# Kernel optimization log

Measured on AMD Instinct MI355X. Metric: run time of the kernel, lower is better.

## Reference

```python
import jax, jax.numpy as jnp
import numpy as np

N_NODES = 100000
N_EDGES = 3200000
IN_DIM = 3
HID = 8
OUT_DIM = 1


def setup_inputs() -> dict:
    key = jax.random.key(0)
    ks = jax.random.split(key, 10)
    x = jax.random.normal(ks[0], (N_NODES, IN_DIM), dtype=jnp.float32)
    edge_index = jax.random.randint(ks[1], (2, N_EDGES), 0, N_NODES, dtype=jnp.int64)
    cat_dim = 2 * (HID + IN_DIM)  # 22
    s = lambda fan_in: 1.0 / np.sqrt(fan_in)
    W_in = jax.random.uniform(ks[2], (IN_DIM, HID), jnp.float32, -s(IN_DIM), s(IN_DIM))
    b_in = jnp.zeros((HID,), jnp.float32)
    W1 = jax.random.uniform(ks[3], (cat_dim, HID), jnp.float32, -s(cat_dim), s(cat_dim))
    b1 = jnp.zeros((HID,), jnp.float32)
    W2 = jax.random.uniform(ks[4], (HID, HID), jnp.float32, -s(HID), s(HID))
    b2 = jnp.zeros((HID,), jnp.float32)
    W_e = jax.random.uniform(ks[5], (cat_dim, OUT_DIM), jnp.float32, -s(cat_dim), s(cat_dim))
    b_e = jnp.zeros((OUT_DIM,), jnp.float32)
    return {"x": x, "edge_index": edge_index, "W_in": W_in, "b_in": b_in,
            "W1": W1, "b1": b1, "W2": W2, "b2": b2, "W_e": W_e, "b_e": b_e}


def reference(x, edge_index, W_in, b_in, W1, b1, W2, b2, W_e, b_e):
    src = edge_index[0]  # j (source)
    dst = edge_index[1]  # i (target)

    # inputnet: Linear + Tanh
    H = jnp.tanh(x @ W_in + b_in)               # [N, HID]
    feat = jnp.concatenate([H, x], axis=-1)      # [N, HID+IN_DIM]

    # One EdgeConv iteration (n_iters=1): message = nn(cat([x_i, x_j - x_i]))
    xi = feat[dst]                                # [E, 11]
    xj = feat[src]                                # [E, 11]
    e = jnp.concatenate([xi, xj - xi], axis=-1)   # [E, 22]
    m = jax.nn.sigmoid(e @ W1 + b1)               # [E, HID]
    m = jax.nn.sigmoid(m @ W2 + b2)               # [E, HID]
    H = jax.ops.segment_sum(m, dst, num_segments=N_NODES)  # scatter-add to targets
    feat = jnp.concatenate([H, x], axis=-1)       # [N, 11]

    # edgenetwork on concatenated endpoint features
    ef = jnp.concatenate([feat[src], feat[dst]], axis=-1)   # [E, 22]
    out = jax.nn.sigmoid(ef @ W_e + b_e)          # [E, 1]
    return out.squeeze(-1)                        # [E]
```

## Files before the change

kernel.cpp:

```cpp
#include <hip/hip_runtime.h>
#include <hip/hip_fp16.h>

#define TPB     256
#define BSH     9
#define BW      512
#define EPB     8192
#define NBMAX   256
#define MAXNB   1024
#define S_SPLIT 8

static __device__ __forceinline__ float sigmoidf(float v) {
    return __builtin_amdgcn_rcpf(1.0f + __expf(-v));
}

static __device__ __forceinline__ void ldgj(const __half* __restrict__ gjh, int n,
                                            float o[8]) {
    uint4 u = *(const uint4*)(gjh + (size_t)n * 8);
    union { unsigned int u; __half2 h; } c0, c1, c2, c3;
    c0.u = u.x; c1.u = u.y; c2.u = u.z; c3.u = u.w;
    float2 f0 = __half22float2(c0.h), f1 = __half22float2(c1.h);
    float2 f2 = __half22float2(c2.h), f3 = __half22float2(c3.h);
    o[0]=f0.x; o[1]=f0.y; o[2]=f1.x; o[3]=f1.y;
    o[4]=f2.x; o[5]=f2.y; o[6]=f3.x; o[7]=f3.y;
}

__global__ void k_feat(const float* __restrict__ x,
                       const float* __restrict__ W_in,
                       const float* __restrict__ b_in,
                       const float* __restrict__ W1,
                       const float* __restrict__ b1,
                       float* __restrict__ gi,
                       __half* __restrict__ gjh, int n_nodes) {
    int t = threadIdx.x;
    int n = blockIdx.x * blockDim.x + t;
    if (n >= n_nodes) return;
    float x0 = x[3*n], x1 = x[3*n+1], x2 = x[3*n+2];
    float f[11];
#pragma unroll
    for (int c = 0; c < 8; ++c)
        f[c] = tanhf(b_in[c] + x0*W_in[c] + x1*W_in[8+c] + x2*W_in[16+c]);
    f[8] = x0; f[9] = x1; f[10] = x2;
    float giv[8], gjv[8];
#pragma unroll
    for (int h = 0; h < 8; ++h) {
        float vi = b1[h], vj = 0.0f;
#pragma unroll
        for (int k = 0; k < 11; ++k) {
            float wa = W1[k*8+h], wb = W1[(11+k)*8+h];
            vi += f[k] * (wa - wb);
            vj += f[k] * wb;
        }
        giv[h] = vi; gjv[h] = vj;
    }
    float4* gip = (float4*)(gi + (size_t)n * 8);
    gip[0] = make_float4(giv[0], giv[1], giv[2], giv[3]);
    gip[1] = make_float4(giv[4], giv[5], giv[6], giv[7]);
    __align__(16) __half hj[8];
#pragma unroll
    for (int k = 0; k < 8; ++k) hj[k] = __float2half_rn(gjv[k]);
    *(uint4*)(gjh + (size_t)n * 8) = *(const uint4*)hj;
}

__global__ void k_hist2(const int* __restrict__ dst, int* __restrict__ raw,
                        int n_edges, int NB) {
    __shared__ int cnt[NBMAX];
    for (int b = threadIdx.x; b < NB; b += blockDim.x) cnt[b] = 0;
    __syncthreads();
    int e0 = blockIdx.x * EPB;
#pragma unroll
    for (int k = 0; k < EPB / (TPB * 4); ++k) {
        int e = e0 + k * TPB * 4 + threadIdx.x * 4;
        if (e + 3 < n_edges) {
            int4 d4 = *(const int4*)(dst + e);
            atomicAdd(&cnt[d4.x >> BSH], 1);
            atomicAdd(&cnt[d4.y >> BSH], 1);
            atomicAdd(&cnt[d4.z >> BSH], 1);
            atomicAdd(&cnt[d4.w >> BSH], 1);
        } else {
            int qe = min(e + 4, n_edges);
            for (int q = e; q < qe; ++q)
                atomicAdd(&cnt[dst[q] >> BSH], 1);
        }
    }
    __syncthreads();
    for (int b = threadIdx.x; b < NB; b += blockDim.x)
        raw[(size_t)blockIdx.x * NB + b] = cnt[b];
}

__global__ void k_scan_cols(const int* __restrict__ raw, int* __restrict__ rel,
                            int* __restrict__ totals, int NB, int NBLK) {
    __shared__ int s[TPB];
    int b = blockIdx.x, t = threadIdx.x;
    int carry = 0;
    for (int q = 0; q < NBLK; q += TPB) {
        int blk = q + t;
        int v = (blk < NBLK) ? raw[(size_t)blk * NB + b] : 0;
        __syncthreads();
        s[t] = v; __syncthreads();
        for (int o = 1; o < TPB; o <<= 1) {
            int u = (t >= o) ? s[t - o] : 0;
            __syncthreads();
            s[t] += u;
            __syncthreads();
        }
        if (blk < NBLK) rel[(size_t)blk * NB + b] = carry + s[t] - v;
        carry += s[TPB - 1];
    }
    if (t == 0) totals[b] = carry;
}

__global__ void k_base(const int* __restrict__ totals, int* __restrict__ base,
                       int NB) {
    __shared__ int s[MAXNB];
    int t = threadIdx.x;
    int v = (t < NB) ? ((totals[t] + 3) & ~3) : 0;
    s[t] = v; __syncthreads();
    for (int o = 1; o < MAXNB; o <<= 1) {
        int u = (t >= o) ? s[t - o] : 0;
        __syncthreads();
        s[t] += u;
        __syncthreads();
    }
    if (t < NB) base[t] = s[t] - v;
}

__launch_bounds__(TPB)
__global__ void k_scatter(const int* __restrict__ src, const int* __restrict__ dst,
                          const int* __restrict__ raw, const int* __restrict__ rel,
                          const int* __restrict__ base,
                          int* __restrict__ sorted, int n_edges, int NB) {
    __shared__ int stage[EPB];
    __shared__ int cnt[NBMAX];
    __shared__ int lscan[NBMAX];
    __shared__ int gd[NBMAX];
    __shared__ int s[TPB];
    int t = threadIdx.x;

    int carry = 0;
    for (int q0 = 0; q0 < NB; q0 += TPB) {
        int idx = q0 + t;
        int v = (idx < NB) ? raw[(size_t)blockIdx.x * NB + idx] : 0;
        __syncthreads();
        s[t] = v; __syncthreads();
        for (int o = 1; o < TPB; o <<= 1) {
            int u = (t >= o) ? s[t - o] : 0;
            __syncthreads();
            s[t] += u;
            __syncthreads();
        }
        if (idx < NB) lscan[idx] = carry + s[t] - v;
        carry += s[TPB - 1];
        __syncthreads();
    }
    for (int b = t; b < NB; b += TPB) {
        cnt[b] = lscan[b];
        gd[b]  = base[b] + rel[(size_t)blockIdx.x * NB + b];
    }
    __syncthreads();

    int e0 = blockIdx.x * EPB;
#pragma unroll
    for (int k = 0; k < EPB / (TPB * 4); ++k) {
        int e = e0 + k * TPB * 4 + t * 4;
        if (e + 3 < n_edges) {
            int4 s4 = *(const int4*)(src + e);
            int4 d4 = *(const int4*)(dst + e);
            int p;
            p = atomicAdd(&cnt[d4.x >> BSH], 1); stage[p] = (s4.x << BSH) | (d4.x & (BW-1));
            p = atomicAdd(&cnt[d4.y >> BSH], 1); stage[p] = (s4.y << BSH) | (d4.y & (BW-1));
            p = atomicAdd(&cnt[d4.z >> BSH], 1); stage[p] = (s4.z << BSH) | (d4.z & (BW-1));
            p = atomicAdd(&cnt[d4.w >> BSH], 1); stage[p] = (s4.w << BSH) | (d4.w & (BW-1));
        } else {
            int qe = min(e + 4, n_edges);
            for (int q = e; q < qe; ++q) {
                int d = dst[q];
                int p = atomicAdd(&cnt[d >> BSH], 1);
                stage[p] = (src[q] << BSH) | (d & (BW - 1));
            }
        }
    }
    __syncthreads();

    int wid = t >> 6, lane = t & 63;
    for (int b = wid; b < NB; b += (TPB / 64)) {
        int ls = lscan[b];
        int le = cnt[b];
        int g0 = gd[b];
        for (int i = ls + lane; i < le; i += 64)
            sorted[g0 + (i - ls)] = stage[i];
    }
}

__launch_bounds__(TPB, 4)
__global__ void k_bucket(const int* __restrict__ sorted, const int* __restrict__ base,
                         const int* __restrict__ totals,
                         const float* __restrict__ gi, const __half* __restrict__ gjh,
                         const float* __restrict__ W2, const float* __restrict__ b2,
                         const float* __restrict__ W_e,
                         float* __restrict__ part, int n_nodes, int NB, int NBP) {
    __shared__ float sa[BW], sc[BW];
    int t = threadIdx.x;
    int sl = blockIdx.x / NBP;
    int b  = blockIdx.x - sl * NBP;
    if (b >= NB) return;

    int nb0 = b * BW;
    for (int i = t; i < BW; i += TPB) { sa[i] = 0.0f; sc[i] = 0.0f; }
    __syncthreads();

    int beg = base[b];
    int len = totals[b];
    int qs = (((len + S_SPLIT - 1) / S_SPLIT) + 3) & ~3;
    int s0 = beg + sl * qs;
    int s1 = min(beg + len, s0 + qs);

    for (int g = s0 + t * 4; g < s1; g += TPB * 4) {
        if (g + 4 <= s1) {
            int4 pp = *(const int4*)(sorted + g);
            int d[4]   = { pp.x & (BW-1), pp.y & (BW-1), pp.z & (BW-1), pp.w & (BW-1) };
            int sj[4]  = { pp.x >> BSH,   pp.y >> BSH,   pp.z >> BSH,   pp.w >> BSH };
            float jv[4][8], iv[4][8];
#pragma unroll
            for (int q = 0; q < 4; ++q) ldgj(gjh, sj[q], jv[q]);
#pragma unroll
            for (int q = 0; q < 4; ++q) {
                const float4* ip = (const float4*)(gi + (size_t)(nb0 + d[q]) * 8);
                float4 A = ip[0], B = ip[1];
                iv[q][0]=A.x; iv[q][1]=A.y; iv[q][2]=A.z; iv[q][3]=A.w;
                iv[q][4]=B.x; iv[q][5]=B.y; iv[q][6]=B.z; iv[q][7]=B.w;
            }
            float m[4][8];
#pragma unroll
            for (int q = 0; q < 4; ++q)
#pragma unroll
                for (int k = 0; k < 8; ++k)
                    m[q][k] = sigmoidf(iv[q][k] + jv[q][k]);
            float pa[4] = {0,0,0,0}, pc[4] = {0,0,0,0};
#pragma unroll
            for (int h = 0; h < 8; ++h) {
                float bb = b2[h];
                float v[4] = {bb, bb, bb, bb};
#pragma unroll
                for (int k = 0; k < 8; ++k) {
                    float w = W2[k*8+h];
#pragma unroll
                    for (int q = 0; q < 4; ++q) v[q] += m[q][k] * w;
                }
                float wa = W_e[h], wc = W_e[11+h];
#pragma unroll
                for (int q = 0; q < 4; ++q) {
                    float z = sigmoidf(v[q]);
                    pa[q] += z * wa; pc[q] += z * wc;
                }
            }
#pragma unroll
            for (int q = 0; q < 4; ++q) {
                atomicAdd(&sa[d[q]], pa[q]);
                atomicAdd(&sc[d[q]], pc[q]);
            }
        } else {
            for (int e = g; e < s1; ++e) {
                int p = sorted[e];
                int dl = p & (BW - 1);
                float jv[8];
                ldgj(gjh, p >> BSH, jv);
                const float4* ip = (const float4*)(gi + (size_t)(nb0 + dl) * 8);
                float4 A = ip[0], B = ip[1];
                float iv[8] = {A.x,A.y,A.z,A.w,B.x,B.y,B.z,B.w};
                float m[8];
#pragma unroll
                for (int k = 0; k < 8; ++k) m[k] = sigmoidf(iv[k] + jv[k]);
                float pa = 0, pc = 0;
#pragma unroll
                for (int h = 0; h < 8; ++h) {
                    float v = b2[h];
#pragma unroll
                    for (int k = 0; k < 8; ++k) v += m[k] * W2[k*8+h];
                    float z = sigmoidf(v);
                    pa += z * W_e[h]; pc += z * W_e[11+h];
                }
                atomicAdd(&sa[dl], pa); atomicAdd(&sc[dl], pc);
            }
        }
    }
    __syncthreads();
    size_t row = (size_t)blockIdx.x * (2 * BW);
    for (int i = t; i < BW; i += TPB) {
        part[row + i]      = sa[i];
        part[row + BW + i] = sc[i];
    }
}

__global__ void k_acc(const float* __restrict__ part, const float* __restrict__ x,
                      const float* __restrict__ W_e, float* __restrict__ ac,
                      int n_nodes, int NBP) {
    int n = blockIdx.x * blockDim.x + threadIdx.x;
    if (n >= n_nodes) return;
    int b = n >> BSH, r = n & (BW - 1);
    float a = 0.0f, c = 0.0f;
#pragma unroll
    for (int s = 0; s < S_SPLIT; ++s) {
        const float* pp = part + ((size_t)(s * NBP + b)) * (2 * BW);
        a += pp[r];
        c += pp[BW + r];
    }
    float x0 = x[3*n], x1 = x[3*n+1], x2 = x[3*n+2];
    a += x0 * W_e[8]  + x1 * W_e[9]  + x2 * W_e[10];
    c += x0 * W_e[19] + x1 * W_e[20] + x2 * W_e[21];
    ac[2*n]     = a;
    ac[2*n + 1] = c;
}

__global__ void k_out2(const int* __restrict__ src, const int* __restrict__ dst,
                       const float* __restrict__ ac, const float* __restrict__ b_e,
                       float* __restrict__ out, int n_edges) {
    float bb = b_e[0];
    int e = (blockIdx.x * blockDim.x + threadIdx.x) * 4;
    if (e + 3 < n_edges) {
        int4 s4 = *(const int4*)(src + e);
        int4 d4 = *(const int4*)(dst + e);
        float4 o;
        o.x = sigmoidf(ac[2*s4.x] + ac[2*d4.x + 1] + bb);
        o.y = sigmoidf(ac[2*s4.y] + ac[2*d4.y + 1] + bb);
        o.z = sigmoidf(ac[2*s4.z] + ac[2*d4.z + 1] + bb);
        o.w = sigmoidf(ac[2*s4.w] + ac[2*d4.w + 1] + bb);
        *(float4*)(out + e) = o;
    } else {
        for (int q = e; q < n_edges; ++q)
            out[q] = sigmoidf(ac[2*src[q]] + ac[2*dst[q] + 1] + bb);
    }
}

__global__ void k_nodes(const float* __restrict__ x, const float* __restrict__ W_in,
                        const float* __restrict__ b_in, float* __restrict__ feat,
                        float* __restrict__ H2, int n_nodes) {
    int i = blockIdx.x * blockDim.x + threadIdx.x;
    if (i >= n_nodes) return;
    float x0 = x[3*i], x1 = x[3*i+1], x2 = x[3*i+2];
    float h[8];
#pragma unroll
    for (int c = 0; c < 8; ++c)
        h[c] = tanhf(b_in[c] + x0*W_in[c] + x1*W_in[8+c] + x2*W_in[16+c]);
    float4* fp = (float4*)(feat + (size_t)i * 12);
    fp[0] = make_float4(h[0],h[1],h[2],h[3]);
    fp[1] = make_float4(h[4],h[5],h[6],h[7]);
    fp[2] = make_float4(x0,x1,x2,0.0f);
    float4* hp = (float4*)(H2 + (size_t)i * 8);
    hp[0] = make_float4(0,0,0,0); hp[1] = make_float4(0,0,0,0);
}

__global__ void k_edges(const int* __restrict__ src, const int* __restrict__ dst,
                        const float* __restrict__ feat, const float* __restrict__ W1,
                        const float* __restrict__ b1, const float* __restrict__ W2,
                        const float* __restrict__ b2, float* __restrict__ H2,
                        int n_edges) {
    __shared__ float sW1[176], sW2[64], sb1[8], sb2[8];
    for (int t = threadIdx.x; t < 176; t += blockDim.x) sW1[t] = W1[t];
    for (int t = threadIdx.x; t < 64;  t += blockDim.x) sW2[t] = W2[t];
    if (threadIdx.x < 8) { sb1[threadIdx.x]=b1[threadIdx.x]; sb2[threadIdx.x]=b2[threadIdx.x]; }
    __syncthreads();
    int e = blockIdx.x * blockDim.x + threadIdx.x;
    if (e >= n_edges) return;
    int j = src[e], i = dst[e];
    const float4* fi = (const float4*)(feat + (size_t)i * 12);
    const float4* fj = (const float4*)(feat + (size_t)j * 12);
    float4 i0=fi[0],i1=fi[1],i2=fi[2],j0=fj[0],j1=fj[1],j2=fj[2];
    float xi[11]={i0.x,i0.y,i0.z,i0.w,i1.x,i1.y,i1.z,i1.w,i2.x,i2.y,i2.z};
    float xj[11]={j0.x,j0.y,j0.z,j0.w,j1.x,j1.y,j1.z,j1.w,j2.x,j2.y,j2.z};
    float dd[11];
#pragma unroll
    for (int k = 0; k < 11; ++k) dd[k]=xj[k]-xi[k];
    float m[8];
#pragma unroll
    for (int h = 0; h < 8; ++h) {
        float v = sb1[h];
#pragma unroll
        for (int k = 0; k < 11; ++k) v += xi[k]*sW1[k*8+h];
#pragma unroll
        for (int k = 0; k < 11; ++k) v += dd[k]*sW1[(11+k)*8+h];
        m[h] = sigmoidf(v);
    }
    float m2[8];
#pragma unroll
    for (int h = 0; h < 8; ++h) {
        float v = sb2[h];
#pragma unroll
        for (int k = 0; k < 8; ++k) v += m[k]*sW2[k*8+h];
        m2[h] = sigmoidf(v);
    }
    float* hp = H2 + (size_t)i * 8;
#pragma unroll
    for (int h = 0; h < 8; ++h) atomicAdd(hp + h, m2[h]);
}

__global__ void k_out(const int* __restrict__ src, const int* __restrict__ dst,
                      const float* __restrict__ H2, const float* __restrict__ x,
                      const float* __restrict__ W_e, const float* __restrict__ b_e,
                      float* __restrict__ out, int n_edges) {
    __shared__ float sW[22]; __shared__ float sb;
    if (threadIdx.x < 22) sW[threadIdx.x] = W_e[threadIdx.x];
    if (threadIdx.x == 0) sb = b_e[0];
    __syncthreads();
    int e = blockIdx.x * blockDim.x + threadIdx.x;
    if (e >= n_edges) return;
    int j = src[e], i = dst[e];
    const float4* hj = (const float4*)(H2 + (size_t)j * 8);
    const float4* hi = (const float4*)(H2 + (size_t)i * 8);
    float4 a0=hj[0],a1=hj[1],c0=hi[0],c1=hi[1];
    float acc = sb;
    acc += a0.x*sW[0]+a0.y*sW[1]+a0.z*sW[2]+a0.w*sW[3];
    acc += a1.x*sW[4]+a1.y*sW[5]+a1.z*sW[6]+a1.w*sW[7];
    acc += x[3*(size_t)j]*sW[8]+x[3*(size_t)j+1]*sW[9]+x[3*(size_t)j+2]*sW[10];
    acc += c0.x*sW[11]+c0.y*sW[12]+c0.z*sW[13]+c0.w*sW[14];
    acc += c1.x*sW[15]+c1.y*sW[16]+c1.z*sW[17]+c1.w*sW[18];
    acc += x[3*(size_t)i]*sW[19]+x[3*(size_t)i+1]*sW[20]+x[3*(size_t)i+2]*sW[21];
    out[e] = sigmoidf(acc);
}

extern "C" void kernel_launch(void* const* d_in, const int* in_sizes, int n_in,
                              void* d_out, int out_size, void* d_ws, size_t ws_size,
                              hipStream_t stream) {
    const float* x    = (const float*)d_in[0];
    const int*   ei   = (const int*)d_in[1];
    const float* W_in = (const float*)d_in[2];
    const float* b_in = (const float*)d_in[3];
    const float* W1   = (const float*)d_in[4];
    const float* b1   = (const float*)d_in[5];
    const float* W2   = (const float*)d_in[6];
    const float* b2   = (const float*)d_in[7];
    const float* W_e  = (const float*)d_in[8];
    const float* b_e  = (const float*)d_in[9];

    const int n_nodes = in_sizes[0] / 3;
    const int n_edges = in_sizes[1] / 2;
    const int* src = ei;
    const int* dst = ei + n_edges;
    float* out = (float*)d_out;

    const int NB   = (n_nodes + BW - 1) >> BSH;
    const int NBP  = (NB + 7) & ~7;
    const int NBLK = (n_edges + EPB - 1) / EPB;

    size_t off = 0;
    auto carve = [&](size_t bytes) { size_t o = off; off += (bytes + 255) & ~(size_t)255; return o; };
    char* ws = (char*)d_ws;
    size_t o_gi     = carve((size_t)n_nodes * 8 * 4);
    size_t o_gjh    = carve((size_t)n_nodes * 8 * 2);
    size_t o_ac     = carve((size_t)n_nodes * 2 * 4);
    size_t o_raw    = carve((size_t)NBLK * NB * 4);
    size_t o_rel    = carve((size_t)NBLK * NB * 4);
    size_t o_totals = carve((size_t)NB * 4);
    size_t o_base   = carve(((size_t)NB + 1) * 4);
    size_t o_sorted = carve(((size_t)n_edges + 4 * NBMAX) * 4);
    size_t o_part   = carve((size_t)NBP * S_SPLIT * 2 * BW * 4);
    bool fast = (off <= ws_size) && (NB <= NBMAX);

    if (fast) {
        float*  gi     = (float*)(ws + o_gi);
        __half* gjh    = (__half*)(ws + o_gjh);
        float*  ac     = (float*)(ws + o_ac);
        int*    raw    = (int*)(ws + o_raw);
        int*    rel    = (int*)(ws + o_rel);
        int*    totals = (int*)(ws + o_totals);
        int*    base   = (int*)(ws + o_base);
        int*    sorted = (int*)(ws + o_sorted);
        float*  part   = (float*)(ws + o_part);

        k_feat     <<<(n_nodes + TPB - 1) / TPB, TPB, 0, stream>>>(x, W_in, b_in, W1, b1, gi, gjh, n_nodes);
        k_hist2    <<<NBLK, TPB, 0, stream>>>(dst, raw, n_edges, NB);
        k_scan_cols<<<NB, TPB, 0, stream>>>(raw, rel, totals, NB, NBLK);
        k_base     <<<1, MAXNB, 0, stream>>>(totals, base, NB);
        k_scatter  <<<NBLK, TPB, 0, stream>>>(src, dst, raw, rel, base, sorted, n_edges, NB);
        k_bucket   <<<NBP * S_SPLIT, TPB, 0, stream>>>(sorted, base, totals, gi, gjh, W2, b2, W_e,
                                                       part, n_nodes, NB, NBP);
        k_acc      <<<(n_nodes + TPB - 1) / TPB, TPB, 0, stream>>>(part, x, W_e, ac, n_nodes, NBP);
        k_out2     <<<(n_edges / 4 + TPB - 1) / TPB + 1, TPB, 0, stream>>>(src, dst, ac, b_e, out, n_edges);
    } else {
        float* feat = (float*)d_ws;
        float* H2   = feat + (size_t)n_nodes * 12;
        k_nodes<<<(n_nodes + TPB - 1) / TPB, TPB, 0, stream>>>(x, W_in, b_in, feat, H2, n_nodes);
        k_edges<<<(n_edges + TPB - 1) / TPB, TPB, 0, stream>>>(src, dst, feat, W1, b1, W2, b2, H2, n_edges);
        k_out  <<<(n_edges + TPB - 1) / TPB, TPB, 0, stream>>>(src, dst, H2, x, W_e, b_e, out, n_edges);
    }
}
```

Before: 121.6 us.

## Precompute exp factors per node and pre-gather source features in a deal pass

Node features now store exp(-gi) and exp(-gj), so the first-layer sigmoid becomes 1/(1+ei*ej) and drops one exp per element. A new k_deal kernel gathers each edge's half-precision source row into a contiguous per-edge array and writes 16-bit local destination indices. k_bucket can then stream these with coalesced loads instead of doing random gathers. The cost is an extra kernel and roughly 18 bytes per edge of extra write and read traffic. The exp product can overflow for large pre-activations, and storing exp(-vj) in fp16 overflows or loses precision. The launch bounds occupancy hint is also relaxed.

```diff
diff --git a/kernel.cpp b/kernel.cpp
--- a/kernel.cpp
+++ b/kernel.cpp
@@ -13,9 +13,7 @@
     return __builtin_amdgcn_rcpf(1.0f + __expf(-v));
 }
 
-static __device__ __forceinline__ void ldgj(const __half* __restrict__ gjh, int n,
-                                            float o[8]) {
-    uint4 u = *(const uint4*)(gjh + (size_t)n * 8);
+static __device__ __forceinline__ void unpack8(uint4 u, float o[8]) {
     union { unsigned int u; __half2 h; } c0, c1, c2, c3;
     c0.u = u.x; c1.u = u.y; c2.u = u.z; c3.u = u.w;
     float2 f0 = __half22float2(c0.h), f1 = __half22float2(c1.h);
@@ -29,8 +27,8 @@
                        const float* __restrict__ b_in,
                        const float* __restrict__ W1,
                        const float* __restrict__ b1,
-                       float* __restrict__ gi,
-                       __half* __restrict__ gjh, int n_nodes) {
+                       float* __restrict__ egi,
+                       __half* __restrict__ egjh, int n_nodes) {
     int t = threadIdx.x;
     int n = blockIdx.x * blockDim.x + t;
     if (n >= n_nodes) return;
@@ -50,15 +48,15 @@
             vi += f[k] * (wa - wb);
             vj += f[k] * wb;
         }
-        giv[h] = vi; gjv[h] = vj;
-    }
-    float4* gip = (float4*)(gi + (size_t)n * 8);
+        giv[h] = __expf(-vi); gjv[h] = __expf(-vj);
+    }
+    float4* gip = (float4*)(egi + (size_t)n * 8);
     gip[0] = make_float4(giv[0], giv[1], giv[2], giv[3]);
     gip[1] = make_float4(giv[4], giv[5], giv[6], giv[7]);
     __align__(16) __half hj[8];
 #pragma unroll
     for (int k = 0; k < 8; ++k) hj[k] = __float2half_rn(gjv[k]);
-    *(uint4*)(gjh + (size_t)n * 8) = *(const uint4*)hj;
+    *(uint4*)(egjh + (size_t)n * 8) = *(const uint4*)hj;
 }
 
 __global__ void k_hist2(const int* __restrict__ dst, int* __restrict__ raw,
@@ -191,10 +189,47 @@
     }
 }
 
-__launch_bounds__(TPB, 4)
-__global__ void k_bucket(const int* __restrict__ sorted, const int* __restrict__ base,
-                         const int* __restrict__ totals,
-                         const float* __restrict__ gi, const __half* __restrict__ gjh,
+__global__ void k_deal(const int* __restrict__ sorted,
+                       const __half* __restrict__ egjh,
+                       __half* __restrict__ gjs,
+                       unsigned short* __restrict__ dls,
+                       int limit, int n_nodes) {
+    int e4 = (blockIdx.x * blockDim.x + threadIdx.x) * 4;
+    if (e4 + 3 < limit) {
+        int4 p = *(const int4*)(sorted + e4);
+        int s0 = p.x >> BSH, s1 = p.y >> BSH, s2 = p.z >> BSH, s3 = p.w >> BSH;
+        if ((unsigned)s0 >= (unsigned)n_nodes) s0 = 0;
+        if ((unsigned)s1 >= (unsigned)n_nodes) s1 = 0;
+        if ((unsigned)s2 >= (unsigned)n_nodes) s2 = 0;
+        if ((unsigned)s3 >= (unsigned)n_nodes) s3 = 0;
+        uint4 v0 = *(const uint4*)(egjh + (size_t)s0 * 8);
+        uint4 v1 = *(const uint4*)(egjh + (size_t)s1 * 8);
+        uint4 v2 = *(const uint4*)(egjh + (size_t)s2 * 8);
+        uint4 v3 = *(const uint4*)(egjh + (size_t)s3 * 8);
+        uint4* gp = (uint4*)(gjs + (size_t)e4 * 8);
+        gp[0] = v0; gp[1] = v1; gp[2] = v2; gp[3] = v3;
+        ushort4 dl4;
+        dl4.x = (unsigned short)(p.x & (BW-1));
+        dl4.y = (unsigned short)(p.y & (BW-1));
+        dl4.z = (unsigned short)(p.z & (BW-1));
+        dl4.w = (unsigned short)(p.w & (BW-1));
+        *(ushort4*)(dls + e4) = dl4;
+    } else {
+        for (int e = e4; e < limit; ++e) {
+            int p = sorted[e];
+            int s = p >> BSH;
+            if ((unsigned)s >= (unsigned)n_nodes) s = 0;
+            *(uint4*)(gjs + (size_t)e * 8) = *(const uint4*)(egjh + (size_t)s * 8);
+            dls[e] = (unsigned short)(p & (BW-1));
+        }
+    }
+}
+
+__launch_bounds__(TPB)
+__global__ void k_bucket(const unsigned short* __restrict__ dls,
+                         const __half* __restrict__ gjs,
+                         const int* __restrict__ base, const int* __restrict__ totals,
+                         const float* __restrict__ egi,
                          const float* __restrict__ W2, const float* __restrict__ b2,
                          const float* __restrict__ W_e,
                          float* __restrict__ part, int n_nodes, int NB, int NBP) {
@@ -216,25 +251,23 @@
 
     for (int g = s0 + t * 4; g < s1; g += TPB * 4) {
         if (g + 4 <= s1) {
-            int4 pp = *(const int4*)(sorted + g);
-            int d[4]   = { pp.x & (BW-1), pp.y & (BW-1), pp.z & (BW-1), pp.w & (BW-1) };
-            int sj[4]  = { pp.x >> BSH,   pp.y >> BSH,   pp.z >> BSH,   pp.w >> BSH };
-            float jv[4][8], iv[4][8];
-#pragma unroll
-            for (int q = 0; q < 4; ++q) ldgj(gjh, sj[q], jv[q]);
+            ushort4 d4 = *(const ushort4*)(dls + g);
+            int d[4] = { d4.x, d4.y, d4.z, d4.w };
+            const uint4* gp = (const uint4*)(gjs + (size_t)g * 8);
+            uint4 u0 = gp[0], u1 = gp[1], u2 = gp[2], u3 = gp[3];
+            float ej[4][8];
+            unpack8(u0, ej[0]); unpack8(u1, ej[1]);
+            unpack8(u2, ej[2]); unpack8(u3, ej[3]);
+            float m[4][8];
 #pragma unroll
             for (int q = 0; q < 4; ++q) {
-                const float4* ip = (const float4*)(gi + (size_t)(nb0 + d[q]) * 8);
+                const float4* ip = (const float4*)(egi + (size_t)(nb0 + d[q]) * 8);
                 float4 A = ip[0], B = ip[1];
-                iv[q][0]=A.x; iv[q][1]=A.y; iv[q][2]=A.z; iv[q][3]=A.w;
-                iv[q][4]=B.x; iv[q][5]=B.y; iv[q][6]=B.z; iv[q][7]=B.w;
+                float ei[8] = {A.x,A.y,A.z,A.w,B.x,B.y,B.z,B.w};
+#pragma unroll
+                for (int k = 0; k < 8; ++k)
+                    m[q][k] = __builtin_amdgcn_rcpf(1.0f + ei[k] * ej[q][k]);
             }
-            float m[4][8];
-#pragma unroll
-            for (int q = 0; q < 4; ++q)
-#pragma unroll
-                for (int k = 0; k < 8; ++k)
-                    m[q][k] = sigmoidf(iv[q][k] + jv[q][k]);
             float pa[4] = {0,0,0,0}, pc[4] = {0,0,0,0};
 #pragma unroll
             for (int h = 0; h < 8; ++h) {
@@ -260,16 +293,16 @@
             }
         } else {
             for (int e = g; e < s1; ++e) {
-                int p = sorted[e];
-                int dl = p & (BW - 1);
-                float jv[8];
-                ldgj(gjh, p >> BSH, jv);
-                const float4* ip = (const float4*)(gi + (size_t)(nb0 + dl) * 8);
+                int dl = dls[e];
+                float ej[8];
+                unpack8(*(const uint4*)(gjs + (size_t)e * 8), ej);
+                const float4* ip = (const float4*)(egi + (size_t)(nb0 + dl) * 8);
                 float4 A = ip[0], B = ip[1];
-                float iv[8] = {A.x,A.y,A.z,A.w,B.x,B.y,B.z,B.w};
+                float ei[8] = {A.x,A.y,A.z,A.w,B.x,B.y,B.z,B.w};
                 float m[8];
 #pragma unroll
-                for (int k = 0; k < 8; ++k) m[k] = sigmoidf(iv[k] + jv[k]);
+                for (int k = 0; k < 8; ++k)
+                    m[k] = __builtin_amdgcn_rcpf(1.0f + ei[k] * ej[k]);
                 float pa = 0, pc = 0;
 #pragma unroll
                 for (int h = 0; h < 8; ++h) {
@@ -437,41 +470,47 @@
     const int* dst = ei + n_edges;
     float* out = (float*)d_out;
 
-    const int NB   = (n_nodes + BW - 1) >> BSH;
-    const int NBP  = (NB + 7) & ~7;
-    const int NBLK = (n_edges + EPB - 1) / EPB;
+    const int NB    = (n_nodes + BW - 1) >> BSH;
+    const int NBP   = (NB + 7) & ~7;
+    const int NBLK  = (n_edges + EPB - 1) / EPB;
+    const int LIMIT = n_edges + 4 * NB;
 
     size_t off = 0;
     auto carve = [&](size_t bytes) { size_t o = off; off += (bytes + 255) & ~(size_t)255; return o; };
     char* ws = (char*)d_ws;
-    size_t o_gi     = carve((size_t)n_nodes * 8 * 4);
-    size_t o_gjh    = carve((size_t)n_nodes * 8 * 2);
+    size_t o_egi    = carve((size_t)n_nodes * 8 * 4);
+    size_t o_egjh   = carve((size_t)n_nodes * 8 * 2);
     size_t o_ac     = carve((size_t)n_nodes * 2 * 4);
     size_t o_raw    = carve((size_t)NBLK * NB * 4);
     size_t o_rel    = carve((size_t)NBLK * NB * 4);
     size_t o_totals = carve((size_t)NB * 4);
     size_t o_base   = carve(((size_t)NB + 1) * 4);
-    size_t o_sorted = carve(((size_t)n_edges + 4 * NBMAX) * 4);
+    size_t o_sorted = carve(((size_t)LIMIT + 4) * 4);
+    size_t o_gjs    = carve(((size_t)LIMIT + 4) * 16);
+    size_t o_dls    = carve(((size_t)LIMIT + 4) * 2);
     size_t o_part   = carve((size_t)NBP * S_SPLIT * 2 * BW * 4);
     bool fast = (off <= ws_size) && (NB <= NBMAX);
 
     if (fast) {
-        float*  gi     = (float*)(ws + o_gi);
-        __half* gjh    = (__half*)(ws + o_gjh);
+        float*  egi    = (float*)(ws + o_egi);
+        __half* egjh   = (__half*)(ws + o_egjh);
         float*  ac     = (float*)(ws + o_ac);
         int*    raw    = (int*)(ws + o_raw);
         int*    rel    = (int*)(ws + o_rel);
         int*    totals = (int*)(ws + o_totals);
         int*    base   = (int*)(ws + o_base);
         int*    sorted = (int*)(ws + o_sorted);
+        __half* gjs    = (__half*)(ws + o_gjs);
+        unsigned short* dls = (unsigned short*)(ws + o_dls);
         float*  part   = (float*)(ws + o_part);
 
-        k_feat     <<<(n_nodes + TPB - 1) / TPB, TPB, 0, stream>>>(x, W_in, b_in, W1, b1, gi, gjh, n_nodes);
+        k_feat     <<<(n_nodes + TPB - 1) / TPB, TPB, 0, stream>>>(x, W_in, b_in, W1, b1, egi, egjh, n_nodes);
         k_hist2    <<<NBLK, TPB, 0, stream>>>(dst, raw, n_edges, NB);
         k_scan_cols<<<NB, TPB, 0, stream>>>(raw, rel, totals, NB, NBLK);
         k_base     <<<1, MAXNB, 0, stream>>>(totals, base, NB);
         k_scatter  <<<NBLK, TPB, 0, stream>>>(src, dst, raw, rel, base, sorted, n_edges, NB);
-        k_bucket   <<<NBP * S_SPLIT, TPB, 0, stream>>>(sorted, base, totals, gi, gjh, W2, b2, W_e,
+        k_deal     <<<(LIMIT / 4 + TPB - 1) / TPB + 1, TPB, 0, stream>>>(sorted, egjh, gjs, dls, LIMIT, n_nodes);
+        k_bucket   <<<NBP * S_SPLIT, TPB, 0, stream>>>(dls, gjs, base, totals, egi, W2, b2, W_e,
                                                        part, n_nodes, NB, NBP);
         k_acc      <<<(n_nodes + TPB - 1) / TPB, TPB, 0, stream>>>(part, x, W_e, ac, n_nodes, NBP);
         k_out2     <<<(n_edges / 4 + TPB - 1) / TPB + 1, TPB, 0, stream>>>(src, dst, ac, b_e, out, n_edges);
```

Measured after the change: 146.6 us. 1.21x slower.
